# Performance work log

Hardware: AMD Instinct MI355X
Metric: run time of the kernel (lower is better)

Reference implementation:

```python
import jax, jax.numpy as jnp
import numpy as np

H = 16      # num_heads
HD = 128    # head_dim
P = 5       # num_paths
STAT = 4
HIDDEN = 2048
GATE_IN = HIDDEN + H * STAT * P + H * P + H * (P * (P - 1) // 2)  # 2608
GATE_HID = HIDDEN // 2  # 1024
OUT_DIM = H * P


def setup_inputs() -> dict:
    key = jax.random.key(0)
    ks = jax.random.split(key, 10)
    B, L = 2, 4096
    inp = {"hidden_states": jax.random.normal(ks[0], (B, L, HIDDEN), jnp.float32)}
    for i in range(P):
        inp[f"p{i}"] = jax.random.normal(ks[1 + i], (B, L, H, HD), jnp.float32)
    # QuantizedLinear treated as standard Linear (torch default init)
    s1 = 1.0 / np.sqrt(GATE_IN)
    s2 = 1.0 / np.sqrt(GATE_HID)
    inp["W1"] = jax.random.uniform(ks[6], (GATE_HID, GATE_IN), jnp.float32, -s1, s1)
    inp["b1"] = jax.random.uniform(ks[7], (GATE_HID,), jnp.float32, -s1, s1)
    inp["W2"] = jax.random.uniform(ks[8], (OUT_DIM, GATE_HID), jnp.float32, -s2, s2)
    # bias init: zero then favor paths 3 (value) and 4 (identity)
    b2 = np.zeros((H, P), np.float32)
    b2[:, 3] = 1.0
    b2[:, 4] = 2.0
    inp["b2"] = jnp.asarray(b2.reshape(-1))
    inp["log_temp"] = jnp.zeros((H, 1), jnp.float32)  # log(temp_init=1.0)
    return inp


def _forward(hidden_states, paths, W1, b1, W2, b2, log_temp):
    B, L, _ = hidden_states.shape
    ps = jnp.stack(paths, axis=-1)  # [B,L,H,D,P]
    # --- per-path stats over head_dim ---
    mean = ps.mean(axis=-2)                      # [B,L,H,P]
    var = ps.var(axis=-2)                        # unbiased=False
    abs_mean = jnp.abs(ps).mean(axis=-2)
    sq = jnp.sum(ps * ps, axis=-2)               # [B,L,H,P]
    l2 = jnp.sqrt(sq)
    stats = jnp.stack([mean, var, abs_mean, l2], axis=-1)   # [B,L,H,P,STAT] -> (p s) order
    stats_flat = stats.reshape(B, L, H, P * STAT)
    norms_flat = l2                                         # [B,L,H,P]
    # --- pairwise L2 distances: ||a-b||^2 = ||a||^2+||b||^2-2<a,b> ---
    dots = jnp.einsum('blhdp,blhdq->blhpq', ps, ps)
    d2 = sq[..., :, None] + sq[..., None, :] - 2.0 * dots
    dist = jnp.sqrt(jnp.clip(d2, 0.0, None))                # [B,L,H,P,P]
    iu0, iu1 = np.triu_indices(P, k=1)
    pairwise = dist[..., iu0, iu1]                           # [B,L,H,P*(P-1)/2]
    # --- router MLP ---
    gate_input = jnp.concatenate([
        hidden_states,
        stats_flat.reshape(B, L, -1),
        norms_flat.reshape(B, L, -1),
        pairwise.reshape(B, L, -1),
    ], axis=-1)  # [B,L,GATE_IN]
    h = jax.nn.gelu(gate_input @ W1.T + b1, approximate=False)
    logits = (h @ W2.T + b2).reshape(B, L, H, P)
    temp = jnp.exp(log_temp)[None, None]                     # [1,1,H,1]
    probs = jax.nn.softmax(logits / temp, axis=-1)
    probs = jnp.clip(probs, 0.02, None)
    probs = probs / probs.sum(axis=-1, keepdims=True)
    output = jnp.einsum('blhdp,blhp->blhd', ps, probs)       # [B,L,H,HD]
    return output


def reference(hidden_states, p0, p1, p2, p3, p4, W1, b1, W2, b2, log_temp):
    out = _forward(hidden_states, [p0, p1, p2, p3, p4], W1, b1, W2, b2, log_temp)
    reg_loss = jnp.float32(0.0)  # eval mode: no entropy regularizer
    return out, reg_loss
```

## Files before the change

kernel.cpp:

```cpp
#include <hip/hip_runtime.h>
#include <hip/hip_bf16.h>
#include <cstdint>
#include <cstddef>

typedef _Float16 half8 __attribute__((ext_vector_type(8)));
typedef _Float16 half4 __attribute__((ext_vector_type(4)));
typedef _Float16 half2v __attribute__((ext_vector_type(2)));
typedef float floatx4 __attribute__((ext_vector_type(4)));

#define KIN   2608
#define KP    2624
#define GH    1024
#define NOUT  80
#define NTOK  8192
#define HID   2048

__device__ __forceinline__ void async_copy16(const void* gsrc, void* ldst) {
  __builtin_amdgcn_global_load_lds(
      (const __attribute__((address_space(1))) void*)gsrc,
      (__attribute__((address_space(3))) void*)ldst, 16, 0, 0);
}

__global__ __launch_bounds__(256) void convertw(
    const float* __restrict__ W1, const float* __restrict__ W2,
    _Float16* __restrict__ W1p, _Float16* __restrict__ W2p)
{
  int i = blockIdx.x * 256 + threadIdx.x;
  const int total1 = GH * KP;
  if (i < total1) {
    int n = i / KP;
    int k = i - n * KP;
    W1p[i] = (k < KIN) ? (_Float16)W1[(size_t)n * KIN + k] : (_Float16)0.f;
  } else {
    int j = i - total1;
    if (j < NOUT * GH) W2p[j] = (_Float16)W2[j];
  }
}

__global__ __launch_bounds__(256) void k1_fused(
    const float* __restrict__ hidden,
    const float* __restrict__ p0, const float* __restrict__ p1,
    const float* __restrict__ p2, const float* __restrict__ p3,
    const float* __restrict__ p4,
    _Float16* __restrict__ gate)
{
  const int wave = threadIdx.x >> 6;
  const int lane = threadIdx.x & 63;
  const int token = blockIdx.x * 4 + wave;
  const int h = lane >> 2;
  const int sub = lane & 3;
  const float* paths[5] = {p0, p1, p2, p3, p4};
  const size_t hb = ((size_t)token * 16 + h) * 128;

  float s[5], s2[5], sa[5], dt[10];
#pragma unroll
  for (int p = 0; p < 5; ++p) { s[p] = 0.f; s2[p] = 0.f; sa[p] = 0.f; }
#pragma unroll
  for (int i = 0; i < 10; ++i) dt[i] = 0.f;

#pragma unroll
  for (int j = 0; j < 8; ++j) {
    const int chunk = sub + j * 4;
    float v[5][4];
#pragma unroll
    for (int p = 0; p < 5; ++p) {
      float4 x = *(const float4*)(paths[p] + hb + chunk * 4);
      v[p][0] = x.x; v[p][1] = x.y; v[p][2] = x.z; v[p][3] = x.w;
    }
#pragma unroll
    for (int p = 0; p < 5; ++p) {
#pragma unroll
      for (int e = 0; e < 4; ++e) {
        float x = v[p][e];
        s[p] += x; s2[p] += x * x; sa[p] += fabsf(x);
      }
    }
    int pi = 0;
#pragma unroll
    for (int a = 0; a < 5; ++a)
#pragma unroll
      for (int b = a + 1; b < 5; ++b) {
        float d = 0.f;
#pragma unroll
        for (int e = 0; e < 4; ++e) d += v[a][e] * v[b][e];
        dt[pi++] += d;
      }
  }

#pragma unroll
  for (int p = 0; p < 5; ++p) {
    s[p]  += __shfl_xor(s[p], 1, 4);  s[p]  += __shfl_xor(s[p], 2, 4);
    s2[p] += __shfl_xor(s2[p], 1, 4); s2[p] += __shfl_xor(s2[p], 2, 4);
    sa[p] += __shfl_xor(sa[p], 1, 4); sa[p] += __shfl_xor(sa[p], 2, 4);
  }
#pragma unroll
  for (int i = 0; i < 10; ++i) {
    dt[i] += __shfl_xor(dt[i], 1, 4); dt[i] += __shfl_xor(dt[i], 2, 4);
  }

  _Float16* gs = gate + (size_t)token * KP;
  if (sub < 2) {
#pragma unroll
    for (int q = 0; q < 2; ++q) {
      int p = sub * 2 + q;
      float mean = s[p] * (1.f / 128.f);
      float var  = s2[p] * (1.f / 128.f) - mean * mean;
      float am   = sa[p] * (1.f / 128.f);
      float l2   = sqrtf(s2[p]);
      half4 st;
      st[0] = (_Float16)mean; st[1] = (_Float16)var;
      st[2] = (_Float16)am;   st[3] = (_Float16)l2;
      *(half4*)(gs + 2048 + h * 20 + p * 4) = st;
    }
  } else if (sub == 2) {
    {
      int p = 4;
      float mean = s[p] * (1.f / 128.f);
      float var  = s2[p] * (1.f / 128.f) - mean * mean;
      float am   = sa[p] * (1.f / 128.f);
      float l2   = sqrtf(s2[p]);
      half4 st;
      st[0] = (_Float16)mean; st[1] = (_Float16)var;
      st[2] = (_Float16)am;   st[3] = (_Float16)l2;
      *(half4*)(gs + 2048 + h * 20 + p * 4) = st;
    }
#pragma unroll
    for (int p = 0; p < 5; ++p) gs[2368 + h * 5 + p] = (_Float16)sqrtf(s2[p]);
  } else {
    float pw[10];
    int pi = 0;
#pragma unroll
    for (int a = 0; a < 5; ++a)
#pragma unroll
      for (int b = a + 1; b < 5; ++b) {
        float d2 = s2[a] + s2[b] - 2.f * dt[pi];
        pw[pi] = sqrtf(fmaxf(d2, 0.f));
        ++pi;
      }
#pragma unroll
    for (int i = 0; i < 5; ++i) {
      half2v t; t[0] = (_Float16)pw[2 * i]; t[1] = (_Float16)pw[2 * i + 1];
      *(half2v*)(gs + 2448 + h * 10 + 2 * i) = t;
    }
    if (h == 0) {
      half8 z = {(_Float16)0.f, (_Float16)0.f, (_Float16)0.f, (_Float16)0.f,
                 (_Float16)0.f, (_Float16)0.f, (_Float16)0.f, (_Float16)0.f};
      *(half8*)(gs + 2608) = z;
      *(half8*)(gs + 2616) = z;
    }
  }

  const float* hrow = hidden + (size_t)token * HID;
#pragma unroll
  for (int j = 0; j < 4; ++j) {
    int c = lane + 64 * j;
    float4 a = *(const float4*)(hrow + c * 8);
    float4 b = *(const float4*)(hrow + c * 8 + 4);
    half8 hv;
    hv[0] = (_Float16)a.x; hv[1] = (_Float16)a.y; hv[2] = (_Float16)a.z; hv[3] = (_Float16)a.w;
    hv[4] = (_Float16)b.x; hv[5] = (_Float16)b.y; hv[6] = (_Float16)b.z; hv[7] = (_Float16)b.w;
    *(half8*)(gs + c * 8) = hv;
  }
}

__global__ __launch_bounds__(256) void gemm1(
    const _Float16* __restrict__ A,
    const _Float16* __restrict__ Bt,
    const float* __restrict__ b1,
    _Float16* __restrict__ Hm)
{
  __shared__ _Float16 As[128 * 64];
  __shared__ _Float16 Bs[128 * 64];
  const int tid  = threadIdx.x;
  const int lane = tid & 63;
  const int wave = tid >> 6;
  const int m0 = blockIdx.x * 128;
  const int n0 = blockIdx.y * 128;
  const int wm = (wave & 1) * 64;
  const int wn = (wave >> 1) * 64;

  floatx4 acc[4][4];
#pragma unroll
  for (int i = 0; i < 4; ++i)
#pragma unroll
    for (int k = 0; k < 4; ++k) acc[i][k] = (floatx4){0.f, 0.f, 0.f, 0.f};

  for (int kt = 0; kt < KP / 64; ++kt) {
    __syncthreads();
    const int kbase = kt * 64;
#pragma unroll
    for (int r = 0; r < 4; ++r) {
      int chunk = r * 256 + tid;
      int row = chunk >> 3;
      int kk  = (chunk & 7) * 8;
      const _Float16* ga = A  + (size_t)(m0 + row) * KP + kbase + kk;
      const _Float16* gb = Bt + (size_t)(n0 + row) * KP + kbase + kk;
      async_copy16(ga, &As[0] + (r * 2048 + wave * 512));
      async_copy16(gb, &Bs[0] + (r * 2048 + wave * 512));
    }
    __syncthreads();
#pragma unroll
    for (int ks = 0; ks < 2; ++ks) {
      half8 af[4], bf[4];
#pragma unroll
      for (int i = 0; i < 4; ++i) {
        int ar = wm + i * 16 + (lane & 15);
        af[i] = *(const half8*)&As[ar * 64 + ks * 32 + (lane >> 4) * 8];
        int br = wn + i * 16 + (lane & 15);
        bf[i] = *(const half8*)&Bs[br * 64 + ks * 32 + (lane >> 4) * 8];
      }
#pragma unroll
      for (int mi = 0; mi < 4; ++mi)
#pragma unroll
        for (int ni = 0; ni < 4; ++ni)
          acc[mi][ni] = __builtin_amdgcn_mfma_f32_16x16x32_f16(af[mi], bf[ni], acc[mi][ni], 0, 0, 0);
    }
  }
#pragma unroll
  for (int mi = 0; mi < 4; ++mi) {
#pragma unroll
    for (int ni = 0; ni < 4; ++ni) {
      int col = n0 + wn + ni * 16 + (lane & 15);
      float bias = b1[col];
#pragma unroll
      for (int r = 0; r < 4; ++r) {
        int row = m0 + wm + mi * 16 + (lane >> 4) * 4 + r;
        float x = acc[mi][ni][r] + bias;
        float g = 0.5f * x * (1.f + erff(x * 0.70710678118654752f));
        Hm[(size_t)row * GH + col] = (_Float16)g;
      }
    }
  }
}

__global__ __launch_bounds__(256) void gemm2(
    const _Float16* __restrict__ Hm, const _Float16* __restrict__ W2p,
    const float* __restrict__ b2, float* __restrict__ logits)
{
  const int lane = threadIdx.x & 63;
  const int wave = threadIdx.x >> 6;
  const int m0 = blockIdx.x * 64 + wave * 16;
  const int mrow = m0 + (lane & 15);
  const int koff = (lane >> 4) * 8;
  floatx4 acc[5];
#pragma unroll
  for (int i = 0; i < 5; ++i) acc[i] = (floatx4){0.f, 0.f, 0.f, 0.f};
  for (int k0 = 0; k0 < GH; k0 += 32) {
    half8 af = *(const half8*)&Hm[(size_t)mrow * GH + k0 + koff];
#pragma unroll
    for (int ni = 0; ni < 5; ++ni) {
      half8 bf = *(const half8*)&W2p[(size_t)(ni * 16 + (lane & 15)) * GH + k0 + koff];
      acc[ni] = __builtin_amdgcn_mfma_f32_16x16x32_f16(af, bf, acc[ni], 0, 0, 0);
    }
  }
#pragma unroll
  for (int ni = 0; ni < 5; ++ni) {
    int col = ni * 16 + (lane & 15);
    float bias = b2[col];
#pragma unroll
    for (int r = 0; r < 4; ++r) {
      int row = m0 + (lane >> 4) * 4 + r;
      logits[(size_t)row * NOUT + col] = acc[ni][r] + bias;
    }
  }
}

__global__ __launch_bounds__(256) void softmaxk(
    const float* __restrict__ logits, const float* __restrict__ log_temp,
    float* __restrict__ probs)
{
  int id = blockIdx.x * 256 + threadIdx.x;
  int t = id >> 4;
  int h = id & 15;
  float it = __expf(-log_temp[h]);
  const float* lp = logits + (size_t)t * NOUT + h * 5;
  float x[5];
  float m = -1e30f;
#pragma unroll
  for (int p = 0; p < 5; ++p) { x[p] = lp[p] * it; m = fmaxf(m, x[p]); }
  float ssum = 0.f;
#pragma unroll
  for (int p = 0; p < 5; ++p) { x[p] = __expf(x[p] - m); ssum += x[p]; }
  float inv = 1.f / ssum;
  float c = 0.f;
#pragma unroll
  for (int p = 0; p < 5; ++p) { x[p] = fmaxf(x[p] * inv, 0.02f); c += x[p]; }
  float inv2 = 1.f / c;
  float* pp = probs + (size_t)t * NOUT + h * 5;
#pragma unroll
  for (int p = 0; p < 5; ++p) pp[p] = x[p] * inv2;
}

__global__ __launch_bounds__(256) void k5_combine(
    const float* __restrict__ p0, const float* __restrict__ p1,
    const float* __restrict__ p2, const float* __restrict__ p3,
    const float* __restrict__ p4,
    const float* __restrict__ probs, float* __restrict__ out)
{
  size_t i4 = (size_t)blockIdx.x * 256 + threadIdx.x;
  int token = (int)(i4 >> 9);
  int rem = (int)(i4 & 511);
  int h = rem >> 5;
  const float* pb = probs + (size_t)token * NOUT + h * 5;
  float w0 = pb[0], w1 = pb[1], w2 = pb[2], w3 = pb[3], w4 = pb[4];
  size_t off = i4 * 4;
  float4 a0 = *(const float4*)(p0 + off);
  float4 a1 = *(const float4*)(p1 + off);
  float4 a2 = *(const float4*)(p2 + off);
  float4 a3 = *(const float4*)(p3 + off);
  float4 a4 = *(const float4*)(p4 + off);
  float4 r;
  r.x = a0.x * w0 + a1.x * w1 + a2.x * w2 + a3.x * w3 + a4.x * w4;
  r.y = a0.y * w0 + a1.y * w1 + a2.y * w2 + a3.y * w3 + a4.y * w4;
  r.z = a0.z * w0 + a1.z * w1 + a2.z * w2 + a3.z * w3 + a4.z * w4;
  r.w = a0.w * w0 + a1.w * w1 + a2.w * w2 + a3.w * w3 + a4.w * w4;
  *(float4*)(out + off) = r;
  if (i4 == 0) out[(size_t)NTOK * 2048] = 0.f;
}

extern "C" void kernel_launch(void* const* d_in, const int* in_sizes, int n_in,
                              void* d_out, int out_size, void* d_ws, size_t ws_size,
                              hipStream_t stream) {
  const float* hidden  = (const float*)d_in[0];
  const float* p0      = (const float*)d_in[1];
  const float* p1      = (const float*)d_in[2];
  const float* p2      = (const float*)d_in[3];
  const float* p3      = (const float*)d_in[4];
  const float* p4      = (const float*)d_in[5];
  const float* W1      = (const float*)d_in[6];
  const float* b1      = (const float*)d_in[7];
  const float* W2      = (const float*)d_in[8];
  const float* b2      = (const float*)d_in[9];
  const float* logtemp = (const float*)d_in[10];
  float* out = (float*)d_out;

  char* ws = (char*)d_ws;
  _Float16* gate = (_Float16*)(ws);
  _Float16* W1p  = (_Float16*)(ws + 42991616);
  _Float16* W2p  = (_Float16*)(ws + 48365568);
  _Float16* Hm   = (_Float16*)(ws + 48529408);
  float*    logits = (float*)(ws + 65306624);
  float*    probs  = (float*)(ws + 67928064);

  convertw<<<10816, 256, 0, stream>>>(W1, W2, W1p, W2p);
  k1_fused<<<2048, 256, 0, stream>>>(hidden, p0, p1, p2, p3, p4, gate);
  gemm1<<<dim3(NTOK / 128, GH / 128), 256, 0, stream>>>(gate, W1p, b1, Hm);
  gemm2<<<NTOK / 64, 256, 0, stream>>>(Hm, W2p, b2, logits);
  softmaxk<<<(NTOK * 16) / 256, 256, 0, stream>>>(logits, logtemp, probs);
  k5_combine<<<(NTOK * 2048 / 4) / 256, 256, 0, stream>>>(p0, p1, p2, p3, p4, probs, out);
}
```

Measured before the change: 564.4 us.

## Stage per-token path data into LDS with async global-to-LDS copies in stats kernel

```diff
diff --git a/kernel.cpp b/kernel.cpp
--- a/kernel.cpp
+++ b/kernel.cpp
@@ -37,20 +37,56 @@
   }
 }
 
-__global__ __launch_bounds__(256) void k1_fused(
+__global__ __launch_bounds__(128) void k1_staged(
     const float* __restrict__ hidden,
     const float* __restrict__ p0, const float* __restrict__ p1,
     const float* __restrict__ p2, const float* __restrict__ p3,
     const float* __restrict__ p4,
     _Float16* __restrict__ gate)
 {
-  const int wave = threadIdx.x >> 6;
-  const int lane = threadIdx.x & 63;
-  const int token = blockIdx.x * 4 + wave;
-  const int h = lane >> 2;
-  const int sub = lane & 3;
+  __shared__ float lds[10240];
+  const int tid  = threadIdx.x;
+  const int wave = tid >> 6;
+  const int lane = tid & 63;
+  const int token = blockIdx.x;
   const float* paths[5] = {p0, p1, p2, p3, p4};
-  const size_t hb = ((size_t)token * 16 + h) * 128;
+
+#pragma unroll
+  for (int r = 0; r < 20; ++r) {
+    int i = r * 2 + wave;
+    int p = i >> 3;
+    int s = i & 7;
+    const float* src = paths[p] + (size_t)token * 2048 + s * 256 + lane * 4;
+    async_copy16(src, (char*)lds + i * 1024);
+  }
+
+  float4 hv[4];
+  const float* hrow = hidden + (size_t)token * HID;
+#pragma unroll
+  for (int j = 0; j < 4; ++j)
+    hv[j] = *(const float4*)(hrow + (j * 128 + tid) * 4);
+
+  __syncthreads();
+
+  _Float16* gs = gate + (size_t)token * KP;
+
+#pragma unroll
+  for (int j = 0; j < 4; ++j) {
+    half4 o;
+    o[0] = (_Float16)hv[j].x; o[1] = (_Float16)hv[j].y;
+    o[2] = (_Float16)hv[j].z; o[3] = (_Float16)hv[j].w;
+    *(half4*)(gs + (j * 128 + tid) * 4) = o;
+  }
+  if (tid == 0) {
+    half8 z = {(_Float16)0.f, (_Float16)0.f, (_Float16)0.f, (_Float16)0.f,
+               (_Float16)0.f, (_Float16)0.f, (_Float16)0.f, (_Float16)0.f};
+    *(half8*)(gs + 2608) = z;
+    *(half8*)(gs + 2616) = z;
+  }
+
+  const int idx  = wave * 64 + lane;
+  const int head = idx >> 3;
+  const int sub  = idx & 7;
 
   float s[5], s2[5], sa[5], dt[10];
 #pragma unroll
@@ -59,12 +95,11 @@
   for (int i = 0; i < 10; ++i) dt[i] = 0.f;
 
 #pragma unroll
-  for (int j = 0; j < 8; ++j) {
-    const int chunk = sub + j * 4;
+  for (int j = 0; j < 4; ++j) {
     float v[5][4];
 #pragma unroll
     for (int p = 0; p < 5; ++p) {
-      float4 x = *(const float4*)(paths[p] + hb + chunk * 4);
+      const float4 x = *(const float4*)&lds[p * 2048 + head * 128 + j * 32 + sub * 4];
       v[p][0] = x.x; v[p][1] = x.y; v[p][2] = x.z; v[p][3] = x.w;
     }
 #pragma unroll
@@ -89,77 +124,41 @@
 
 #pragma unroll
   for (int p = 0; p < 5; ++p) {
-    s[p]  += __shfl_xor(s[p], 1, 4);  s[p]  += __shfl_xor(s[p], 2, 4);
-    s2[p] += __shfl_xor(s2[p], 1, 4); s2[p] += __shfl_xor(s2[p], 2, 4);
-    sa[p] += __shfl_xor(sa[p], 1, 4); sa[p] += __shfl_xor(sa[p], 2, 4);
+    s[p]  += __shfl_xor(s[p], 1, 8);  s[p]  += __shfl_xor(s[p], 2, 8);  s[p]  += __shfl_xor(s[p], 4, 8);
+    s2[p] += __shfl_xor(s2[p], 1, 8); s2[p] += __shfl_xor(s2[p], 2, 8); s2[p] += __shfl_xor(s2[p], 4, 8);
+    sa[p] += __shfl_xor(sa[p], 1, 8); sa[p] += __shfl_xor(sa[p], 2, 8); sa[p] += __shfl_xor(sa[p], 4, 8);
   }
 #pragma unroll
   for (int i = 0; i < 10; ++i) {
-    dt[i] += __shfl_xor(dt[i], 1, 4); dt[i] += __shfl_xor(dt[i], 2, 4);
-  }
-
-  _Float16* gs = gate + (size_t)token * KP;
-  if (sub < 2) {
-#pragma unroll
-    for (int q = 0; q < 2; ++q) {
-      int p = sub * 2 + q;
-      float mean = s[p] * (1.f / 128.f);
-      float var  = s2[p] * (1.f / 128.f) - mean * mean;
-      float am   = sa[p] * (1.f / 128.f);
-      float l2   = sqrtf(s2[p]);
-      half4 st;
-      st[0] = (_Float16)mean; st[1] = (_Float16)var;
-      st[2] = (_Float16)am;   st[3] = (_Float16)l2;
-      *(half4*)(gs + 2048 + h * 20 + p * 4) = st;
-    }
-  } else if (sub == 2) {
-    {
-      int p = 4;
-      float mean = s[p] * (1.f / 128.f);
-      float var  = s2[p] * (1.f / 128.f) - mean * mean;
-      float am   = sa[p] * (1.f / 128.f);
-      float l2   = sqrtf(s2[p]);
-      half4 st;
-      st[0] = (_Float16)mean; st[1] = (_Float16)var;
-      st[2] = (_Float16)am;   st[3] = (_Float16)l2;
-      *(half4*)(gs + 2048 + h * 20 + p * 4) = st;
-    }
-#pragma unroll
-    for (int p = 0; p < 5; ++p) gs[2368 + h * 5 + p] = (_Float16)sqrtf(s2[p]);
+    dt[i] += __shfl_xor(dt[i], 1, 8); dt[i] += __shfl_xor(dt[i], 2, 8); dt[i] += __shfl_xor(dt[i], 4, 8);
+  }
+
+  if (sub < 5) {
+    int p = sub;
+    float mean = s[p] * (1.f / 128.f);
+    float var  = s2[p] * (1.f / 128.f) - mean * mean;
+    float am   = sa[p] * (1.f / 128.f);
+    float l2   = sqrtf(s2[p]);
+    half4 st;
+    st[0] = (_Float16)mean; st[1] = (_Float16)var;
+    st[2] = (_Float16)am;   st[3] = (_Float16)l2;
+    *(half4*)(gs + 2048 + head * 20 + p * 4) = st;
+  } else if (sub == 5) {
+#pragma unroll
+    for (int p = 0; p < 5; ++p) gs[2368 + head * 5 + p] = (_Float16)sqrtf(s2[p]);
   } else {
-    float pw[10];
+    int lo = (sub == 6) ? 0 : 5;
     int pi = 0;
 #pragma unroll
     for (int a = 0; a < 5; ++a)
 #pragma unroll
       for (int b = a + 1; b < 5; ++b) {
-        float d2 = s2[a] + s2[b] - 2.f * dt[pi];
-        pw[pi] = sqrtf(fmaxf(d2, 0.f));
+        if (pi >= lo && pi < lo + 5) {
+          float d2 = s2[a] + s2[b] - 2.f * dt[pi];
+          gs[2448 + head * 10 + pi] = (_Float16)sqrtf(fmaxf(d2, 0.f));
+        }
         ++pi;
       }
-#pragma unroll
-    for (int i = 0; i < 5; ++i) {
-      half2v t; t[0] = (_Float16)pw[2 * i]; t[1] = (_Float16)pw[2 * i + 1];
-      *(half2v*)(gs + 2448 + h * 10 + 2 * i) = t;
-    }
-    if (h == 0) {
-      half8 z = {(_Float16)0.f, (_Float16)0.f, (_Float16)0.f, (_Float16)0.f,
-                 (_Float16)0.f, (_Float16)0.f, (_Float16)0.f, (_Float16)0.f};
-      *(half8*)(gs + 2608) = z;
-      *(half8*)(gs + 2616) = z;
-    }
-  }
-
-  const float* hrow = hidden + (size_t)token * HID;
-#pragma unroll
-  for (int j = 0; j < 4; ++j) {
-    int c = lane + 64 * j;
-    float4 a = *(const float4*)(hrow + c * 8);
-    float4 b = *(const float4*)(hrow + c * 8 + 4);
-    half8 hv;
-    hv[0] = (_Float16)a.x; hv[1] = (_Float16)a.y; hv[2] = (_Float16)a.z; hv[3] = (_Float16)a.w;
-    hv[4] = (_Float16)b.x; hv[5] = (_Float16)b.y; hv[6] = (_Float16)b.z; hv[7] = (_Float16)b.w;
-    *(half8*)(gs + c * 8) = hv;
   }
 }
 
@@ -343,7 +342,7 @@
   float*    probs  = (float*)(ws + 67928064);
 
   convertw<<<10816, 256, 0, stream>>>(W1, W2, W1p, W2p);
-  k1_fused<<<2048, 256, 0, stream>>>(hidden, p0, p1, p2, p3, p4, gate);
+  k1_staged<<<NTOK, 128, 0, stream>>>(hidden, p0, p1, p2, p3, p4, gate);
   gemm1<<<dim3(NTOK / 128, GH / 128), 256, 0, stream>>>(gate, W1p, b1, Hm);
   gemm2<<<NTOK / 64, 256, 0, stream>>>(Hm, W2p, b2, logits);
   softmaxk<<<(NTOK * 16) / 256, 256, 0, stream>>>(logits, logtemp, probs);
```

Result: no change. 559.4 us (-0.9%).
